# Kernel tuning notes

Measured on AMD Instinct MI355X. Metric: run time of the kernel, lower is better.

The kernel has to match this reference:

```python
import jax, jax.numpy as jnp
import numpy as np

B, S, N, H, V = 8, 512, 32, 256, 100001
NEG = -1e9
SLOPE = 0.2  # LeakyReLU negative slope


def setup_inputs() -> dict:
    key = jax.random.key(0)
    k1, k2, k3, k4, k5 = jax.random.split(key, 5)
    node_ids = jax.random.randint(k1, (B, S), 0, V)
    neighs = jax.random.randint(k2, (B, S, N), 0, V)
    mask = jax.random.randint(k3, (B, S, N, 1), 0, 2).astype(jnp.int32)
    emb_table = jax.random.normal(k4, (V, H), dtype=jnp.float32) * 0.02
    a_w = jax.random.normal(k5, (2 * H, 1), dtype=jnp.float32) * (1.0 / np.sqrt(2 * H))
    a_b = jnp.zeros((1,), dtype=jnp.float32)
    return {"node_ids": node_ids, "neighs": neighs, "mask": mask,
            "emb_table": emb_table, "a_w": a_w, "a_b": a_b}


def reference(node_ids, neighs, mask, emb_table, a_w, a_b):
    # Gather embeddings
    src = emb_table[node_ids][:, :, None, :]          # [B,S,1,H]
    nbr = emb_table[neighs]                           # [B,S,N,H]
    neigh_embs = jnp.concatenate([src, nbr], axis=2)  # [B,S,N+1,H] (self + neighbors)
    # Concat src with each candidate -> [B,S,N+1,2H]
    src_rep = jnp.broadcast_to(src, neigh_embs.shape)
    embs = jnp.concatenate([src_rep, neigh_embs], axis=-1)
    # Tiny linear (2H -> 1) + LeakyReLU(0.2)
    z = embs @ a_w + a_b                              # [B,S,N+1,1]
    att = jnp.where(z > 0, z, SLOPE * z)
    # Mask neighbor slots (self at index 0 is never masked)
    att = att.at[:, :, 1:].add(mask.astype(att.dtype) * NEG)
    w = jax.nn.softmax(att, axis=2)                   # [B,S,N+1,1]
    # Weighted aggregate: w^T @ neigh_embs
    out = jnp.sum(w * neigh_embs, axis=2)             # [B,S,H]
    return out
```

## Files before the change

### kernel.cpp

```cpp
#include <hip/hip_runtime.h>
#include <math.h>


constexpr int H  = 256;
constexpr int NN = 32;
constexpr int C  = NN + 1;
constexpr int PF = 16;
constexpr float SLOPE = 0.2f;

__device__ __forceinline__ float wave_sum(float v) {
#pragma unroll
  for (int off = 32; off > 0; off >>= 1)
    v += __shfl_xor(v, off, 64);
  return v;
}

__global__ __launch_bounds__(256, 4) void gat_kernel(
    const int*   __restrict__ node_ids,
    const int*   __restrict__ neighs,
    const int*   __restrict__ mask,
    const float* __restrict__ emb,
    const float* __restrict__ a_w,
    const float* __restrict__ a_b,
    float*       __restrict__ out,
    int npos)
{
  __shared__ int slds[4][64];

  const int wid  = (blockIdx.x * blockDim.x + threadIdx.x) >> 6;
  const int wv   = (threadIdx.x >> 6);
  const int lane = threadIdx.x & 63;
  if (wid >= npos) return;
  const int l4 = lane << 2;

  const float4 aw1 = *(const float4*)(a_w + l4);
  const float4 aw2 = *(const float4*)(a_w + H + l4);
  const float  ab  = a_b[0];

  bool active = false;
  int  my_idx = 0;
  if (lane == 0) {
    my_idx = node_ids[wid];
    active = true;
  } else if (lane <= NN) {
    my_idx = neighs[wid * NN + lane - 1];
    active = (mask[wid * NN + lane - 1] == 0);
  }

  const unsigned long long bal = __ballot(active);
  const int K = __popcll(bal);
  if (active) {
    const int rank = (int)__popcll(bal & ((1ull << lane) - 1ull));
    slds[wv][rank] = my_idx;
  }
  const int cidx = slds[wv][lane];

  const float4* __restrict__ embv = (const float4*)emb;
  auto rowbase = [&](int c) -> const float4* {
    const int ic = __builtin_amdgcn_readlane(cidx, c);
    return embv + (size_t)ic * (H / 4);
  };

  float4 buf[PF];
#pragma unroll
  for (int i = 0; i < PF; ++i)
    if (i < K) buf[i] = rowbase(i)[lane];

  float  m = -1e30f, s = 0.f, zsrc = 0.f;
  float4 acc = {0.f, 0.f, 0.f, 0.f};

#pragma unroll
  for (int c = 0; c < C; ++c) {
    if (c < K) {
      const float4 cur = buf[c & (PF - 1)];
      if (c + PF < K) buf[c & (PF - 1)] = rowbase(c + PF)[lane];

      float p = cur.x * aw2.x + cur.y * aw2.y + cur.z * aw2.z + cur.w * aw2.w;
      if (c == 0) {
        float ps = cur.x * aw1.x + cur.y * aw1.y + cur.z * aw1.z + cur.w * aw1.w;
        zsrc = wave_sum(ps);
      }
      const float z = zsrc + wave_sum(p) + ab;
      const float a = (z > 0.f) ? z : SLOPE * z;

      const float mnew  = fmaxf(m, a);
      const float scale = __expf(m - mnew);
      const float pr    = __expf(a - mnew);
      s = s * scale + pr;
      acc.x = acc.x * scale + pr * cur.x;
      acc.y = acc.y * scale + pr * cur.y;
      acc.z = acc.z * scale + pr * cur.z;
      acc.w = acc.w * scale + pr * cur.w;
      m = mnew;
    }
  }

  const float inv = 1.f / s;
  float4 o = {acc.x * inv, acc.y * inv, acc.z * inv, acc.w * inv};
  *(float4*)(out + (size_t)wid * H + l4) = o;
}

extern "C" void kernel_launch(void* const* d_in, const int* in_sizes, int n_in,
                              void* d_out, int out_size, void* d_ws, size_t ws_size,
                              hipStream_t stream) {
  const int*   node_ids = (const int*)d_in[0];
  const int*   neighs   = (const int*)d_in[1];
  const int*   mask     = (const int*)d_in[2];
  const float* emb      = (const float*)d_in[3];
  const float* a_w      = (const float*)d_in[4];
  const float* a_b      = (const float*)d_in[5];
  float*       out      = (float*)d_out;

  const int npos = in_sizes[0];
  const int waves_per_block = 256 / 64;
  const int grid = (npos + waves_per_block - 1) / waves_per_block;

  gat_kernel<<<grid, 256, 0, stream>>>(node_ids, neighs, mask, emb, a_w, a_b,
                                       out, npos);
}
```

Before: 158.8 us.

## Split each position's candidate rows across four waves with LDS softmax merge

Each block now handles one position, and its four waves take the compacted candidate rows in round-robin order. Each wave keeps a partial online-softmax state, and wave 0 merges the four partial states through LDS. This cuts the serial chain of loads and reductions per wave and issues all row loads up front. In exchange it adds two block barriers and an LDS merge step per position, and waves 1-3 sit idle while wave 0 merges.

```diff
diff --git a/kernel.cpp b/kernel.cpp
--- a/kernel.cpp
+++ b/kernel.cpp
@@ -2,10 +2,11 @@
 #include <math.h>
 
 
-constexpr int H  = 256;
-constexpr int NN = 32;
-constexpr int C  = NN + 1;
-constexpr int PF = 16;
+constexpr int H    = 256;
+constexpr int NN   = 32;
+constexpr int C    = NN + 1;
+constexpr int WPB  = 4;
+constexpr int JMAX = (C + WPB - 1) / WPB;
 constexpr float SLOPE = 0.2f;
 
 __device__ __forceinline__ float wave_sum(float v) {
@@ -15,74 +16,78 @@
   return v;
 }
 
-__global__ __launch_bounds__(256, 4) void gat_kernel(
+__global__ __launch_bounds__(256, 5) void gat_kernel(
     const int*   __restrict__ node_ids,
     const int*   __restrict__ neighs,
     const int*   __restrict__ mask,
     const float* __restrict__ emb,
     const float* __restrict__ a_w,
     const float* __restrict__ a_b,
-    float*       __restrict__ out,
-    int npos)
+    float*       __restrict__ out)
 {
-  __shared__ int slds[4][64];
+  __shared__ int    sidx[64];
+  __shared__ int    sKs;
+  __shared__ float  smx[WPB], ssum[WPB];
+  __shared__ float4 sacc[WPB][64];
 
-  const int wid  = (blockIdx.x * blockDim.x + threadIdx.x) >> 6;
-  const int wv   = (threadIdx.x >> 6);
+  const int pos  = blockIdx.x;
+  const int wv   = threadIdx.x >> 6;
   const int lane = threadIdx.x & 63;
-  if (wid >= npos) return;
-  const int l4 = lane << 2;
+  const int l4   = lane << 2;
+
+  if (wv == 0) {
+    bool active = false;
+    int  my     = 0;
+    if (lane == 0) {
+      my = node_ids[pos];
+      active = true;
+    } else if (lane <= NN) {
+      my     = neighs[pos * NN + lane - 1];
+      active = (mask[pos * NN + lane - 1] == 0);
+    }
+    const unsigned long long bal = __ballot(active);
+    if (active)
+      sidx[(int)__popcll(bal & ((1ull << lane) - 1ull))] = my;
+    if (lane == 0) sKs = (int)__popcll(bal);
+  }
+  __syncthreads();
+
+  const int K    = __builtin_amdgcn_readfirstlane(sKs);
+  const int cidx = sidx[lane];
+  const int swv  = __builtin_amdgcn_readfirstlane(wv);
 
   const float4 aw1 = *(const float4*)(a_w + l4);
   const float4 aw2 = *(const float4*)(a_w + H + l4);
   const float  ab  = a_b[0];
+  const float4* __restrict__ embv = (const float4*)emb;
 
-  bool active = false;
-  int  my_idx = 0;
-  if (lane == 0) {
-    my_idx = node_ids[wid];
-    active = true;
-  } else if (lane <= NN) {
-    my_idx = neighs[wid * NN + lane - 1];
-    active = (mask[wid * NN + lane - 1] == 0);
+  const int    iself = __builtin_amdgcn_readlane(cidx, 0);
+  const float4 es    = embv[(size_t)iself * (H / 4) + lane];
+
+  float4 buf[JMAX];
+#pragma unroll
+  for (int j = 0; j < JMAX; ++j) {
+    const int c = swv + WPB * j;
+    if (c < K) {
+      const int ic = __builtin_amdgcn_readlane(cidx, c);
+      buf[j] = embv[(size_t)ic * (H / 4) + lane];
+    }
   }
 
-  const unsigned long long bal = __ballot(active);
-  const int K = __popcll(bal);
-  if (active) {
-    const int rank = (int)__popcll(bal & ((1ull << lane) - 1ull));
-    slds[wv][rank] = my_idx;
-  }
-  const int cidx = slds[wv][lane];
+  const float zsrc = wave_sum(es.x * aw1.x + es.y * aw1.y +
+                              es.z * aw1.z + es.w * aw1.w);
 
-  const float4* __restrict__ embv = (const float4*)emb;
-  auto rowbase = [&](int c) -> const float4* {
-    const int ic = __builtin_amdgcn_readlane(cidx, c);
-    return embv + (size_t)ic * (H / 4);
-  };
-
-  float4 buf[PF];
+  float  m = -1e30f, s = 0.f;
+  float4 acc = {0.f, 0.f, 0.f, 0.f};
 #pragma unroll
-  for (int i = 0; i < PF; ++i)
-    if (i < K) buf[i] = rowbase(i)[lane];
-
-  float  m = -1e30f, s = 0.f, zsrc = 0.f;
-  float4 acc = {0.f, 0.f, 0.f, 0.f};
-
-#pragma unroll
-  for (int c = 0; c < C; ++c) {
+  for (int j = 0; j < JMAX; ++j) {
+    const int c = swv + WPB * j;
     if (c < K) {
-      const float4 cur = buf[c & (PF - 1)];
-      if (c + PF < K) buf[c & (PF - 1)] = rowbase(c + PF)[lane];
-
-      float p = cur.x * aw2.x + cur.y * aw2.y + cur.z * aw2.z + cur.w * aw2.w;
-      if (c == 0) {
-        float ps = cur.x * aw1.x + cur.y * aw1.y + cur.z * aw1.z + cur.w * aw1.w;
-        zsrc = wave_sum(ps);
-      }
-      const float z = zsrc + wave_sum(p) + ab;
+      const float4 cur = buf[j];
+      const float  p   = wave_sum(cur.x * aw2.x + cur.y * aw2.y +
+                                  cur.z * aw2.z + cur.w * aw2.w);
+      const float z = zsrc + p + ab;
       const float a = (z > 0.f) ? z : SLOPE * z;
-
       const float mnew  = fmaxf(m, a);
       const float scale = __expf(m - mnew);
       const float pr    = __expf(a - mnew);
@@ -95,9 +100,25 @@
     }
   }
 
-  const float inv = 1.f / s;
-  float4 o = {acc.x * inv, acc.y * inv, acc.z * inv, acc.w * inv};
-  *(float4*)(out + (size_t)wid * H + l4) = o;
+  sacc[wv][lane] = acc;
+  if (lane == 0) { smx[wv] = m; ssum[wv] = s; }
+  __syncthreads();
+
+  if (wv == 0) {
+    const float M = fmaxf(fmaxf(smx[0], smx[1]), fmaxf(smx[2], smx[3]));
+    float  S = 0.f;
+    float4 o = {0.f, 0.f, 0.f, 0.f};
+#pragma unroll
+    for (int w = 0; w < WPB; ++w) {
+      const float f = __expf(smx[w] - M);
+      S += ssum[w] * f;
+      const float4 a = sacc[w][lane];
+      o.x += f * a.x; o.y += f * a.y; o.z += f * a.z; o.w += f * a.w;
+    }
+    const float inv = 1.f / S;
+    o.x *= inv; o.y *= inv; o.z *= inv; o.w *= inv;
+    *(float4*)(out + (size_t)pos * H + l4) = o;
+  }
 }
 
 extern "C" void kernel_launch(void* const* d_in, const int* in_sizes, int n_in,
@@ -112,9 +133,6 @@
   float*       out      = (float*)d_out;
 
   const int npos = in_sizes[0];
-  const int waves_per_block = 256 / 64;
-  const int grid = (npos + waves_per_block - 1) / waves_per_block;
-
-  gat_kernel<<<grid, 256, 0, stream>>>(node_ids, neighs, mask, emb, a_w, a_b,
-                                       out, npos);
+  gat_kernel<<<npos, 256, 0, stream>>>(node_ids, neighs, mask, emb, a_w, a_b,
+                                       out);
 }
```

After: 152.1 us. 1.04x faster.
